# Optimization experiments

Measured on AMD Instinct MI355X. Metric: run time of the kernel, lower is better.

Reference implementation:

```python
import jax, jax.numpy as jnp
import numpy as np

GROUPS = 32
EPS = 1e-6

def groupnorm(x, gamma, beta):
    b, c, h, w = x.shape
    xg = x.reshape(b, GROUPS, c // GROUPS, h, w)
    mean = xg.mean(axis=(2, 3, 4), keepdims=True)
    var = xg.var(axis=(2, 3, 4), keepdims=True)
    xn = ((xg - mean) * jax.lax.rsqrt(var + EPS)).reshape(b, c, h, w)
    return xn * gamma[None, :, None, None] + beta[None, :, None, None]

def conv1x1(x, W, b):
    # x: [b,c,h,w], W: [out,in], b: [out]
    return jnp.einsum('bchw,oc->bohw', x, W) + b[None, :, None, None]

def setup_inputs() -> dict:
    key = jax.random.key(0)
    ks = jax.random.split(key, 12)
    C = 512
    B, H, W = 4, 64, 64
    scale = 1.0 / np.sqrt(C)
    inp = {
        'x': jax.random.normal(ks[0], (B, C, H, W), jnp.float32),
        'mask': jax.random.randint(ks[1], (B, H * W), 0, 2).astype(jnp.float32),
        'gamma': jnp.ones((C,), jnp.float32),
        'beta': jnp.zeros((C,), jnp.float32),
        'Wq': jax.random.normal(ks[2], (C, C), jnp.float32) * scale,
        'bq': jnp.zeros((C,), jnp.float32),
        'Wk': jax.random.normal(ks[3], (C, C), jnp.float32) * scale,
        'bk': jnp.zeros((C,), jnp.float32),
        'Wv': jax.random.normal(ks[4], (C, C), jnp.float32) * scale,
        'bv': jnp.zeros((C,), jnp.float32),
        'Wo': jax.random.normal(ks[5], (C, C), jnp.float32) * scale,
        'bo': jnp.zeros((C,), jnp.float32),
    }
    return inp

def reference(x, mask, gamma, beta, Wq, bq, Wk, bk, Wv, bv, Wo, bo):
    b, c, h, w = x.shape
    hn = groupnorm(x, gamma, beta)
    q = conv1x1(hn, Wq, bq).reshape(b, c, h * w)
    k = conv1x1(hn, Wk, bk).reshape(b, c, h * w)
    v = conv1x1(hn, Wv, bv).reshape(b, c, h * w)
    # scores: [b, hw(query), hw(key)]
    scores = jnp.einsum('bcq,bck->bqk', q, k) * (c ** -0.5)
    attn = jax.nn.softmax(scores, axis=-1)
    # post-softmax multiplicative mask over keys, then renormalize (reweight=True)
    attn = attn * mask[:, None, :]
    attn = attn / jnp.sum(attn, axis=-1, keepdims=True)
    out = jnp.einsum('bck,bqk->bcq', v, attn).reshape(b, c, h, w)
    out = conv1x1(out, Wo, bo)
    return x + out
```

## Files before the change

kernel.cpp:

```cpp
#include <hip/hip_runtime.h>
#include <hip/hip_bf16.h>
#include <stdint.h>

typedef __attribute__((ext_vector_type(4))) float f32x4;
typedef __attribute__((ext_vector_type(16))) float f32x16;
typedef __attribute__((ext_vector_type(4))) int i32x4;
typedef __attribute__((ext_vector_type(8))) int i32x8;
typedef long long ll64;
typedef __attribute__((ext_vector_type(2))) long long ll64x2;

__device__ __forceinline__ float fast_exp2(float x){
#if __has_builtin(__builtin_amdgcn_exp2f)
  return __builtin_amdgcn_exp2f(x);
#else
  return exp2f(x);
#endif
}
__device__ __forceinline__ unsigned char f2fp8(float f){
#if __has_builtin(__builtin_amdgcn_cvt_pk_fp8_f32)
  int r = __builtin_amdgcn_cvt_pk_fp8_f32(f, f, 0, false);
  return (unsigned char)(r & 0xff);
#else
  uint32_t u = __builtin_bit_cast(uint32_t, f);
  uint32_t s = (u >> 24) & 0x80u;
  uint32_t a = u & 0x7fffffffu;
  float af = __builtin_bit_cast(float, a);
  if (af >= 448.f) return (unsigned char)(s | 0x7e);
  a += 0x000fffffu + ((a >> 20) & 1u);
  int e = (int)(a >> 23) - 127;
  if (e < -6) return (unsigned char)s;
  return (unsigned char)(s | (uint32_t)((e + 7) << 3) | ((a >> 20) & 7u));
#endif
}
__device__ __forceinline__ uint32_t pack4(float a, float b, float c, float d){
#if __has_builtin(__builtin_amdgcn_cvt_pk_fp8_f32)
  int lo = __builtin_amdgcn_cvt_pk_fp8_f32(a, b, 0, false);
  int r  = __builtin_amdgcn_cvt_pk_fp8_f32(c, d, lo, true);
  return (uint32_t)r;
#else
  return (uint32_t)f2fp8(a) | ((uint32_t)f2fp8(b) << 8) |
         ((uint32_t)f2fp8(c) << 16) | ((uint32_t)f2fp8(d) << 24);
#endif
}
__device__ __forceinline__ int perm64(int c){
  return (c & ~63) | (((c >> 3) & 3) << 4) | (((c >> 5) & 1) << 3) | (c & 7);
}
__device__ __forceinline__ void gl_lds16b(const unsigned char* g, unsigned char* l){
  __builtin_amdgcn_global_load_lds(
      (const __attribute__((address_space(1))) uint32_t*)g,
      (__attribute__((address_space(3))) uint32_t*)l, 16, 0, 0);
}

__device__ __forceinline__ f32x16 mfma8_32x32x64(i32x8 a, i32x8 b, f32x16 c){
#if __has_builtin(__builtin_amdgcn_mfma_scale_f32_32x32x64_f8f6f4)
  return __builtin_amdgcn_mfma_scale_f32_32x32x64_f8f6f4(a, b, c, 0, 0,
                                                         0, 0x7f7f7f7f, 0, 0x7f7f7f7f);
#else
  ll64x2 al = __builtin_bit_cast(ll64x2, *(i32x4*)&a);
  ll64x2 ah; ah[0] = ((ll64*)&a)[2]; ah[1] = ((ll64*)&a)[3];
  ll64x2 bl = __builtin_bit_cast(ll64x2, *(i32x4*)&b);
  ll64x2 bh; bh[0] = ((ll64*)&b)[2]; bh[1] = ((ll64*)&b)[3];
  c = __builtin_amdgcn_mfma_f32_32x32x16_fp8_fp8(al[0], bl[0], c, 0, 0, 0);
  c = __builtin_amdgcn_mfma_f32_32x32x16_fp8_fp8(al[1], bl[1], c, 0, 0, 0);
  c = __builtin_amdgcn_mfma_f32_32x32x16_fp8_fp8(ah[0], bh[0], c, 0, 0, 0);
  c = __builtin_amdgcn_mfma_f32_32x32x16_fp8_fp8(ah[1], bh[1], c, 0, 0, 0);
  return c;
#endif
}

__global__ __launch_bounds__(256) void k_prep(const float* __restrict__ x,
                                              float* __restrict__ part,
                                              const float* __restrict__ Wq, const float* __restrict__ Wk,
                                              const float* __restrict__ Wv, const float* __restrict__ Wo,
                                              unsigned char* __restrict__ oqk,
                                              unsigned char* __restrict__ ov,
                                              unsigned char* __restrict__ oo){
  __shared__ float red[8];
  const int bid = blockIdx.x;
  if (bid < 1024) {
    const float* p = x + (size_t)bid * 8192;
    float s = 0.f, ss = 0.f;
    for (int i = threadIdx.x; i < 2048; i += 256) {
      float4 v = *(const float4*)(p + (size_t)i * 4);
      s  += v.x + v.y + v.z + v.w;
      ss += v.x*v.x + v.y*v.y + v.z*v.z + v.w*v.w;
    }
    for (int off = 32; off; off >>= 1) { s += __shfl_down(s, off); ss += __shfl_down(ss, off); }
    int w = threadIdx.x >> 6;
    if ((threadIdx.x & 63) == 0) { red[w] = s; red[w + 4] = ss; }
    __syncthreads();
    if (threadIdx.x == 0) {
      part[bid * 2]     = red[0] + red[1] + red[2] + red[3];
      part[bid * 2 + 1] = red[4] + red[5] + red[6] + red[7];
    }
  } else {
    const int cb = bid - 1024;
    const int sel = cb >> 7;
    const float* in = sel == 0 ? Wq : sel == 1 ? Wk : sel == 2 ? Wv : Wo;
    unsigned char* out = sel == 0 ? oqk : sel == 1 ? (oqk + 262144) : sel == 2 ? ov : oo;
    const int i = ((cb & 127) * 256 + threadIdx.x) * 8;
    const int row = i >> 9;
    const int c0  = i & 511;
    float4 v0 = *(const float4*)&in[i];
    float4 v1 = *(const float4*)&in[i + 4];
    unsigned char o[8];
    o[0]=f2fp8(v0.x); o[1]=f2fp8(v0.y); o[2]=f2fp8(v0.z); o[3]=f2fp8(v0.w);
    o[4]=f2fp8(v1.x); o[5]=f2fp8(v1.y); o[6]=f2fp8(v1.z); o[7]=f2fp8(v1.w);
    *(ll64*)&out[row * 512 + perm64(c0)] = *(ll64*)o;
  }
}

__global__ __launch_bounds__(256) void gn_apply(const float* __restrict__ x,
                                                const float* __restrict__ spart,
                                                const float* __restrict__ gamma,
                                                const float* __restrict__ beta,
                                                unsigned char* __restrict__ hn8){
  __shared__ float tile[64][33];
  const int b  = blockIdx.z;
  const int c0 = blockIdx.y * 64;
  const int p0 = blockIdx.x * 32;
  const int t  = threadIdx.x;
  const float* xb = x + (size_t)b * 512 * 4096;
  const int lpx = t & 31, lcc = t >> 5;
#pragma unroll
  for (int i = 0; i < 8; i++)
    tile[lcc + i * 8][lpx] = xb[(size_t)(c0 + lcc + i * 8) * 4096 + p0 + lpx];
  __syncthreads();
  unsigned char* hb = hn8 + (size_t)b * 4096 * 512;
  const int c   = c0 + (t & 31) * 2;
  const int pxi = t >> 5;
  const int g2  = b * 32 + (c >> 4);
  float sum = 0.f, ssum = 0.f;
#pragma unroll
  for (int i = 0; i < 8; i++) { sum += spart[(g2 * 8 + i) * 2]; ssum += spart[(g2 * 8 + i) * 2 + 1]; }
  const float mean = sum * (1.f / 65536.f);
  const float rstd = rsqrtf(ssum * (1.f / 65536.f) - mean * mean + 1e-6f);
  const float ga0 = gamma[c], be0 = beta[c];
  const float ga1 = gamma[c + 1], be1 = beta[c + 1];
  const int cp = perm64(c);
#pragma unroll
  for (int i = 0; i < 4; i++) {
    const int px = pxi + i * 8;
    float v0 = tile[(t & 31) * 2][px];
    float v1 = tile[(t & 31) * 2 + 1][px];
    unsigned int b0 = f2fp8((v0 - mean) * rstd * ga0 + be0);
    unsigned int b1 = f2fp8((v1 - mean) * rstd * ga1 + be1);
    *(unsigned short*)&hb[(size_t)(p0 + px) * 512 + cp] = (unsigned short)(b0 | (b1 << 8));
  }
}

template<int MODE>
__device__ __forceinline__ void gemm8_body(
    int wg, unsigned char* smem,
    const unsigned char* __restrict__ A, const unsigned char* __restrict__ B,
    unsigned char* __restrict__ C8, float* __restrict__ OUTF,
    const float* __restrict__ auxA, const float* __restrict__ auxB,
    const float* __restrict__ partial,
    int K, int ldA, int ldB,
    size_t sA, size_t sB, int gx, int gy)
{
  unsigned char* As = smem;
  unsigned char* Bs = smem + 16384;

  const int bx = wg % gx;
  const int t2 = wg / gx;
  const int by = t2 % gy;
  const int bz = t2 / gy;

  const unsigned char* Ab = A + (size_t)bz * sA;
  const unsigned char* Bb = B + (size_t)bz * sB;
  const int brow = bx * 128;
  const int bcol = by * 128;
  const int t = threadIdx.x;
  const int lane = t & 63;
  const int wid = t >> 6;
  const int wr = wid >> 2;
  const int wc = wid & 3;
  const int l31 = lane & 31;
  const int lh  = lane >> 5;

  f32x16 acc[2];
#pragma unroll
  for (int m = 0; m < 2; m++)
#pragma unroll
    for (int e = 0; e < 16; e++) acc[m][e] = 0.f;

  const unsigned char* srcA1;
  const unsigned char* srcB1;
  {
    const int r = t >> 2, s = (t & 3) ^ ((r >> 1) & 3);
    srcA1 = Ab + (size_t)(brow + r) * ldA + s * 16;
    srcB1 = Bb + (size_t)(bcol + r) * ldB + s * 16;
  }
  auto STAGE = [&](int kt, int buf) {
    const int ko = kt * 64;
    gl_lds16b(srcA1 + ko, &As[buf * 8192 + t * 16]);
    gl_lds16b(srcB1 + ko, &Bs[buf * 8192 + t * 16]);
  };
  auto LDA32 = [&](int buf, int mb) -> i32x8 {
    const int ru = wr * 64 + mb * 32 + l31;
    const int x = (ru >> 1) & 3;
    const unsigned char* base = &As[buf * 8192 + ru * 64];
    i32x4 lo = *(const i32x4*)&base[((2 * lh) ^ x) * 16];
    i32x4 hi = *(const i32x4*)&base[((2 * lh + 1) ^ x) * 16];
    i32x8 r;
    r[0]=lo[0]; r[1]=lo[1]; r[2]=lo[2]; r[3]=lo[3];
    r[4]=hi[0]; r[5]=hi[1]; r[6]=hi[2]; r[7]=hi[3];
    return r;
  };
  auto LDB32 = [&](int buf) -> i32x8 {
    const int ru = wc * 32 + l31;
    const int x = (ru >> 1) & 3;
    const unsigned char* base = &Bs[buf * 8192 + ru * 64];
    i32x4 lo = *(const i32x4*)&base[((2 * lh) ^ x) * 16];
    i32x4 hi = *(const i32x4*)&base[((2 * lh + 1) ^ x) * 16];
    i32x8 r;
    r[0]=lo[0]; r[1]=lo[1]; r[2]=lo[2]; r[3]=lo[3];
    r[4]=hi[0]; r[5]=hi[1]; r[6]=hi[2]; r[7]=hi[3];
    return r;
  };

  const int nk = K >> 6;
  STAGE(0, 0);
  for (int j = 0; j < nk; ++j) {
    const int bi = j & 1;
    asm volatile("s_waitcnt vmcnt(0)" ::: "memory");
    __builtin_amdgcn_s_barrier();
    __builtin_amdgcn_sched_barrier(0);
    if (j + 1 < nk) STAGE(j + 1, bi ^ 1);
    i32x8 aq[2], bq;
    bq = LDB32(bi);
#pragma unroll
    for (int m = 0; m < 2; m++) aq[m] = LDA32(bi, m);
    asm volatile("s_waitcnt lgkmcnt(0)" ::: "memory");
    __builtin_amdgcn_sched_barrier(0);
    __builtin_amdgcn_s_setprio(1);
#pragma unroll
    for (int m = 0; m < 2; m++)
      acc[m] = mfma8_32x32x64(aq[m], bq, acc[m]);
    __builtin_amdgcn_s_setprio(0);
    __builtin_amdgcn_sched_barrier(0);
  }

  const int rowbase = brow + wr * 64;
  const int colbase = bcol + wc * 32;
  const int col = colbase + l31;

  if (MODE == 1) {
    const int tok = col;
#pragma unroll
    for (int mb = 0; mb < 2; mb++)
#pragma unroll
      for (int g = 0; g < 4; g++) {
        const int ch0 = rowbase + mb * 32 + g * 8 + 4 * lh;
        const float* bp = (ch0 < 512) ? (auxA + ch0) : (auxB + ch0 - 512);
        const float4 b4 = *(const float4*)bp;
        unsigned char* dst = C8 + (ch0 < 512 ? 0 : (size_t)8388608);
        const int cp = perm64(ch0 & 511);
        uint32_t w = pack4(acc[mb][g*4+0] + b4.x, acc[mb][g*4+1] + b4.y,
                           acc[mb][g*4+2] + b4.z, acc[mb][g*4+3] + b4.w);
        *(uint32_t*)&dst[(size_t)tok * 512 + cp] = w;
      }
  } else if (MODE == 2) {
    const float bcv = auxA[col];
#pragma unroll
    for (int mb = 0; mb < 2; mb++)
#pragma unroll
      for (int g = 0; g < 4; g++) {
        const int t0 = rowbase + mb * 32 + g * 8 + 4 * lh;
        const int bb = t0 >> 12, p0 = t0 & 4095;
        uint32_t w = pack4(acc[mb][g*4+0] + bcv, acc[mb][g*4+1] + bcv,
                           acc[mb][g*4+2] + bcv, acc[mb][g*4+3] + bcv);
        *(uint32_t*)&C8[((size_t)bb * 512 + col) * 4096 + perm64(p0)] = w;
      }
  } else if (MODE == 4) {
    float* rtmp  = (float*)(smem + 32768);
    float* rinvL = (float*)(smem + 32768 + 2048);
    {
      const int row = t >> 2, q4 = t & 3;
      const float* pb = partial + ((size_t)bz * 32 + q4 * 8) * 4096 + (bcol + row);
      float s = 0.f;
#pragma unroll
      for (int i = 0; i < 8; i++) s += pb[(size_t)i * 4096];
      rtmp[row * 4 + q4] = s;
    }
    __syncthreads();
    if (t < 128) rinvL[t] = 1.f / (rtmp[t * 4] + rtmp[t * 4 + 1] + rtmp[t * 4 + 2] + rtmp[t * 4 + 3]);
    __syncthreads();
    const int ql = wc * 32 + l31;
    const float ri = rinvL[ql];
    const size_t tok = (size_t)bz * 4096 + bcol + ql;
#pragma unroll
    for (int mb = 0; mb < 2; mb++)
#pragma unroll
      for (int g = 0; g < 4; g++) {
        const int c0 = rowbase + mb * 32 + g * 8 + 4 * lh;
        uint32_t w = pack4(acc[mb][g*4+0] * ri, acc[mb][g*4+1] * ri,
                           acc[mb][g*4+2] * ri, acc[mb][g*4+3] * ri);
        *(uint32_t*)&C8[tok * 512 + perm64(c0)] = w;
      }
  } else {
    const float bv = auxB[col];
#pragma unroll
    for (int mb = 0; mb < 2; mb++)
#pragma unroll
      for (int g = 0; g < 4; g++) {
        const int r0 = rowbase + mb * 32 + g * 8 + 4 * lh;
        const int bb = r0 >> 12;
        const int p  = r0 & 4095;
        const size_t idx = ((size_t)bb * 512 + col) * 4096 + p;
        const float4 xv = *(const float4*)&auxA[idx];
        float4 ov;
        ov.x = acc[mb][g * 4 + 0] + xv.x + bv;
        ov.y = acc[mb][g * 4 + 1] + xv.y + bv;
        ov.z = acc[mb][g * 4 + 2] + xv.z + bv;
        ov.w = acc[mb][g * 4 + 3] + xv.w + bv;
        *(float4*)&OUTF[idx] = ov;
      }
  }
}

__global__ __launch_bounds__(512, 2)
void k_qkv(const unsigned char* __restrict__ hn8, const unsigned char* __restrict__ Wqk8,
           const unsigned char* __restrict__ Wv8,
           unsigned char* __restrict__ qk8, unsigned char* __restrict__ vcm8,
           const float* __restrict__ bq, const float* __restrict__ bk,
           const float* __restrict__ bv){
  __shared__ __align__(16) unsigned char SMEM[32768];
  const int lin = blockIdx.x;
  const int nwg = gridDim.x;
  const int wg = ((lin & 7) * (nwg >> 3)) + (lin >> 3);
  if (wg < 1024)
    gemm8_body<1>(wg, SMEM, Wqk8, hn8, qk8, nullptr, bq, bk, nullptr,
                  512, 512, 512, 0, 0, 8, 128);
  else
    gemm8_body<2>(wg - 1024, SMEM, hn8, Wv8, vcm8, nullptr, bv, nullptr, nullptr,
                  512, 512, 512, 0, 0, 128, 4);
}

__global__ __launch_bounds__(512, 2)
void k_pv(const unsigned char* __restrict__ vcm8, const unsigned char* __restrict__ P8,
          unsigned char* __restrict__ ot8, const float* __restrict__ partial){
  __shared__ __align__(16) unsigned char SMEM[32768 + 2560];
  const int lin = blockIdx.x;
  const int nwg = gridDim.x;
  const int wg = ((lin & 7) * (nwg >> 3)) + (lin >> 3);
  gemm8_body<4>(wg, SMEM, vcm8, P8, ot8, nullptr, nullptr, nullptr, partial,
                4096, 4096, 4096,
                (size_t)512 * 4096, (size_t)4096 * 4096, 4, 32);
}
__global__ __launch_bounds__(512, 2)
void k_oproj(const unsigned char* __restrict__ ot8, const unsigned char* __restrict__ Wo8,
             float* __restrict__ out, const float* __restrict__ resid,
             const float* __restrict__ bo){
  __shared__ __align__(16) unsigned char SMEM[32768];
  const int lin = blockIdx.x;
  const int nwg = gridDim.x;
  const int wg = ((lin & 7) * (nwg >> 3)) + (lin >> 3);
  gemm8_body<5>(wg, SMEM, ot8, Wo8, nullptr, out, resid, bo, nullptr,
                512, 512, 512, 0, 0, 128, 4);
}

__global__ __launch_bounds__(512, 2)
void k_scores(const unsigned char* __restrict__ Kt, const unsigned char* __restrict__ Qt,
              unsigned char* __restrict__ C, const float* __restrict__ mask,
              float* __restrict__ partial, float scale,
              size_t sA, size_t sB, size_t sC, int gx, int gy)
{
  __shared__ __align__(16) unsigned char LDSBUF[65536];
  unsigned char* As = LDSBUF;
  unsigned char* Bs = LDSBUF + 32768;

  const int lin = blockIdx.x;
  const int nwg = gridDim.x;
  const int wg = ((lin & 7) * (nwg >> 3)) + (lin >> 3);
  const int bx = wg % gx;
  const int t2 = wg / gx;
  const int by = t2 % gy;
  const int bz = t2 / gy;

  const unsigned char* Ab = Kt + (size_t)bz * sA;
  const unsigned char* Bb = Qt + (size_t)bz * sB;
  const int brow = bx * 256;
  const int bcol = by * 256;
  const int t = threadIdx.x;
  const int lane = t & 63;
  const int wid = t >> 6;
  const int wr = wid >> 2;
  const int wc = wid & 3;
  const int l31 = lane & 31;
  const int lh  = lane >> 5;

  f32x16 acc[4][2];
#pragma unroll
  for (int m = 0; m < 4; m++)
#pragma unroll
    for (int n = 0; n < 2; n++)
#pragma unroll
      for (int e = 0; e < 16; e++) acc[m][n][e] = 0.f;

  const unsigned char* srcA[2];
  const unsigned char* srcB[2];
#pragma unroll
  for (int c = 0; c < 2; ++c) {
    const int q = c * 512 + t, r = q >> 2, s = (q & 3) ^ ((r >> 1) & 3);
    srcA[c] = Ab + (size_t)(brow + r) * 512 + s * 16;
    srcB[c] = Bb + (size_t)(bcol + r) * 512 + s * 16;
  }
  auto STAGE = [&](int kt, int buf) {
    const int ko = kt * 64;
#pragma unroll
    for (int c = 0; c < 2; ++c) {
      gl_lds16b(srcA[c] + ko, &As[buf * 16384 + (c * 512 + t) * 16]);
      gl_lds16b(srcB[c] + ko, &Bs[buf * 16384 + (c * 512 + t) * 16]);
    }
  };
  auto LDA32 = [&](int buf, int mb) -> i32x8 {
    const int ru = wr * 128 + mb * 32 + l31;
    const int x = (ru >> 1) & 3;
    const unsigned char* base = &As[buf * 16384 + ru * 64];
    i32x4 lo = *(const i32x4*)&base[((2 * lh) ^ x) * 16];
    i32x4 hi = *(const i32x4*)&base[((2 * lh + 1) ^ x) * 16];
    i32x8 r;
    r[0]=lo[0]; r[1]=lo[1]; r[2]=lo[2]; r[3]=lo[3];
    r[4]=hi[0]; r[5]=hi[1]; r[6]=hi[2]; r[7]=hi[3];
    return r;
  };
  auto LDB32 = [&](int buf, int nb) -> i32x8 {
    const int ru = wc * 64 + nb * 32 + l31;
    const int x = (ru >> 1) & 3;
    const unsigned char* base = &Bs[buf * 16384 + ru * 64];
    i32x4 lo = *(const i32x4*)&base[((2 * lh) ^ x) * 16];
    i32x4 hi = *(const i32x4*)&base[((2 * lh + 1) ^ x) * 16];
    i32x8 r;
    r[0]=lo[0]; r[1]=lo[1]; r[2]=lo[2]; r[3]=lo[3];
    r[4]=hi[0]; r[5]=hi[1]; r[6]=hi[2]; r[7]=hi[3];
    return r;
  };

  const int nk = 8;
  STAGE(0, 0);
  for (int j = 0; j < nk; ++j) {
    const int bi = j & 1;
    asm volatile("s_waitcnt vmcnt(0)" ::: "memory");
    __builtin_amdgcn_s_barrier();
    __builtin_amdgcn_sched_barrier(0);
    if (j + 1 < nk) STAGE(j + 1, bi ^ 1);
    i32x8 aq[4], bq[2];
#pragma unroll
    for (int n = 0; n < 2; n++) bq[n] = LDB32(bi, n);
#pragma unroll
    for (int m = 0; m < 4; m++) aq[m] = LDA32(bi, m);
    asm volatile("s_waitcnt lgkmcnt(0)" ::: "memory");
    __builtin_amdgcn_sched_barrier(0);
    __builtin_amdgcn_s_setprio(1);
#pragma unroll
    for (int m = 0; m < 4; m++)
#pragma unroll
      for (int n = 0; n < 2; n++)
        acc[m][n] = mfma8_32x32x64(aq[m], bq[n], acc[m][n]);
    __builtin_amdgcn_s_setprio(0);
    __builtin_amdgcn_sched_barrier(0);
  }

  const float* maskb = mask + (size_t)bz * 4096;
  const float sc2 = scale * 1.4426950408889634f;

  asm volatile("s_waitcnt lgkmcnt(0)" ::: "memory");
  __builtin_amdgcn_s_barrier();

  float rs0 = 0.f, rs1 = 0.f;
#pragma unroll
  for (int mi = 0; mi < 4; mi++) {
#pragma unroll
    for (int g = 0; g < 4; g++) {
      const int kl0 = wr * 128 + mi * 32 + g * 8 + 4 * lh;
      const float4 m4 = *(const float4*)&maskb[brow + kl0];
      const int kp = perm64(kl0);
#pragma unroll
      for (int ni = 0; ni < 2; ni++) {
        const int reg = g * 4;
        float v0 = m4.x * fast_exp2(acc[mi][ni][reg + 0] * sc2);
        float v1 = m4.y * fast_exp2(acc[mi][ni][reg + 1] * sc2);
        float v2 = m4.z * fast_exp2(acc[mi][ni][reg + 2] * sc2);
        float v3 = m4.w * fast_exp2(acc[mi][ni][reg + 3] * sc2);
        if (ni == 0) rs0 += v0 + v1 + v2 + v3; else rs1 += v0 + v1 + v2 + v3;
        const int ql = wc * 64 + ni * 32 + l31;
        *(uint32_t*)&LDSBUF[ql * 256 + (kp ^ ((ql & 15) << 4))] = pack4(v0, v1, v2, v3);
      }
    }
  }
  rs0 += __shfl_xor(rs0, 32);
  rs1 += __shfl_xor(rs1, 32);
  if (lh == 0) {
    float* pslot = partial + ((size_t)bz * 32 + (size_t)(bx * 2 + wr)) * 4096;
    pslot[bcol + wc * 64 + l31]      = rs0;
    pslot[bcol + wc * 64 + 32 + l31] = rs1;
  }
  __builtin_amdgcn_s_barrier();
  unsigned char* Cb = C + (size_t)bz * sC;
#pragma unroll
  for (int i = 0; i < 8; i++) {
    const int ch = i * 512 + t;
    const int rl = ch >> 4;
    const int c16 = (ch & 15) * 16;
    i32x4 v = *(const i32x4*)&LDSBUF[rl * 256 + (c16 ^ ((rl & 15) << 4))];
    *(i32x4*)&Cb[(size_t)(bcol + rl) * 4096 + brow + c16] = v;
  }
}

extern "C" void kernel_launch(void* const* d_in, const int* in_sizes, int n_in,
                              void* d_out, int out_size, void* d_ws, size_t ws_size,
                              hipStream_t stream) {
  const float* x     = (const float*)d_in[0];
  const float* mask  = (const float*)d_in[1];
  const float* gamma = (const float*)d_in[2];
  const float* beta  = (const float*)d_in[3];
  const float* Wq    = (const float*)d_in[4];
  const float* bq    = (const float*)d_in[5];
  const float* Wk    = (const float*)d_in[6];
  const float* bk    = (const float*)d_in[7];
  const float* Wv    = (const float*)d_in[8];
  const float* bv    = (const float*)d_in[9];
  const float* Wo    = (const float*)d_in[10];
  const float* bo    = (const float*)d_in[11];
  float* out = (float*)d_out;

  size_t off = 0;
  auto nxt = [&](size_t bytes) -> void* {
    void* p = (char*)d_ws + off;
    off += (bytes + 255) & ~(size_t)255;
    return p;
  };
  float* spart          = (float*)nxt(2048 * sizeof(float));
  float* partial        = (float*)nxt((size_t)4 * 32 * 4096 * 4);
  unsigned char* Wqk8   = (unsigned char*)nxt((size_t)1024 * 512);
  unsigned char* Wv8    = (unsigned char*)nxt((size_t)512 * 512);
  unsigned char* Wo8    = (unsigned char*)nxt((size_t)512 * 512);
  unsigned char* hn8    = (unsigned char*)nxt((size_t)16384 * 512);
  unsigned char* qk8    = (unsigned char*)nxt((size_t)2 * 16384 * 512);
  unsigned char* vcm8   = (unsigned char*)nxt((size_t)4 * 512 * 4096);
  unsigned char* ot8    = (unsigned char*)nxt((size_t)16384 * 512);
  unsigned char* P8     = (unsigned char*)nxt((size_t)4 * 4096 * 4096);

  k_prep<<<1536, 256, 0, stream>>>(x, spart, Wq, Wk, Wv, Wo, Wqk8, Wv8, Wo8);
  gn_apply<<<dim3(128, 8, 4), 256, 0, stream>>>(x, spart, gamma, beta, hn8);
  k_qkv<<<1536, 512, 0, stream>>>(hn8, Wqk8, Wv8, qk8, vcm8, bq, bk, bv);
  k_scores<<<1024, 512, 0, stream>>>(qk8 + (size_t)8388608, qk8, P8, mask, partial,
                                     0.044194173824159216f,
                                     (size_t)4096 * 512, (size_t)4096 * 512,
                                     (size_t)4096 * 4096, 16, 16);
  k_pv<<<512, 512, 0, stream>>>(vcm8, P8, ot8, partial);
  k_oproj<<<512, 512, 0, stream>>>(ot8, Wo8, out, x, bo);
}
```

Measured before the change: 166.6 us.

## Stage GEMM epilogue outputs through LDS for coalesced 16-byte stores

The fp8 GEMM epilogues for QKV, V and PV now write packed results into a swizzled LDS tile. After a barrier, each thread emits one 16-byte row-contiguous global store, replacing scattered 4-byte writes. The output projection swaps its operand order so each lane owns a token column, which makes the fp32 residual read and output write coalesced across lanes. This adds LDS traffic and barriers in the epilogue and relies on the reused shared buffer being free after the main loop.

Measured after the change: 149.4 us (median of 3 runs). 10.3% less time.

```diff
diff --git a/kernel.cpp b/kernel.cpp
--- a/kernel.cpp
+++ b/kernel.cpp
@@ -242,37 +242,57 @@
     __builtin_amdgcn_sched_barrier(0);
   }
 
-  const int rowbase = brow + wr * 64;
-  const int colbase = bcol + wc * 32;
-  const int col = colbase + l31;
+  const int lcol = wc * 32 + l31;
 
   if (MODE == 1) {
-    const int tok = col;
+    asm volatile("s_waitcnt lgkmcnt(0)" ::: "memory");
+    __builtin_amdgcn_s_barrier();
 #pragma unroll
     for (int mb = 0; mb < 2; mb++)
 #pragma unroll
       for (int g = 0; g < 4; g++) {
-        const int ch0 = rowbase + mb * 32 + g * 8 + 4 * lh;
-        const float* bp = (ch0 < 512) ? (auxA + ch0) : (auxB + ch0 - 512);
-        const float4 b4 = *(const float4*)bp;
-        unsigned char* dst = C8 + (ch0 < 512 ? 0 : (size_t)8388608);
-        const int cp = perm64(ch0 & 511);
+        const int lch0 = wr * 64 + mb * 32 + g * 8 + 4 * lh;
+        const int ch0 = brow + lch0;
+        const float4 b4 = *(const float4*)((ch0 < 512) ? (auxA + ch0) : (auxB + ch0 - 512));
+        const int cpL = perm64(lch0 & 127) | (lch0 & 64);
         uint32_t w = pack4(acc[mb][g*4+0] + b4.x, acc[mb][g*4+1] + b4.y,
                            acc[mb][g*4+2] + b4.z, acc[mb][g*4+3] + b4.w);
-        *(uint32_t*)&dst[(size_t)tok * 512 + cp] = w;
+        *(uint32_t*)&smem[lcol * 128 + ((cpL & 127) ^ ((lcol & 7) << 4))] = w;
       }
+    __builtin_amdgcn_s_barrier();
+    unsigned char* dst = C8 + (brow < 512 ? 0 : (size_t)8388608);
+    const int chb = brow & 511;
+#pragma unroll
+    for (int i = 0; i < 2; i++) {
+      const int ch = i * 512 + t;
+      const int rl = ch >> 3, c16 = (ch & 7) * 16;
+      i32x4 v = *(const i32x4*)&smem[rl * 128 + (c16 ^ ((rl & 7) << 4))];
+      *(i32x4*)&dst[(size_t)(bcol + rl) * 512 + chb + c16] = v;
+    }
   } else if (MODE == 2) {
-    const float bcv = auxA[col];
+    const float bcv = auxA[bcol + lcol];
+    asm volatile("s_waitcnt lgkmcnt(0)" ::: "memory");
+    __builtin_amdgcn_s_barrier();
 #pragma unroll
     for (int mb = 0; mb < 2; mb++)
 #pragma unroll
       for (int g = 0; g < 4; g++) {
-        const int t0 = rowbase + mb * 32 + g * 8 + 4 * lh;
-        const int bb = t0 >> 12, p0 = t0 & 4095;
+        const int lt0 = wr * 64 + mb * 32 + g * 8 + 4 * lh;
+        const int ppL = perm64(lt0 & 63) | (lt0 & 64);
         uint32_t w = pack4(acc[mb][g*4+0] + bcv, acc[mb][g*4+1] + bcv,
                            acc[mb][g*4+2] + bcv, acc[mb][g*4+3] + bcv);
-        *(uint32_t*)&C8[((size_t)bb * 512 + col) * 4096 + perm64(p0)] = w;
+        *(uint32_t*)&smem[lcol * 128 + (ppL ^ ((lcol & 7) << 4))] = w;
       }
+    __builtin_amdgcn_s_barrier();
+    const int bb = brow >> 12;
+    const int pb = brow & 4095;
+#pragma unroll
+    for (int i = 0; i < 2; i++) {
+      const int ch = i * 512 + t;
+      const int rl = ch >> 3, c16 = (ch & 7) * 16;
+      i32x4 v = *(const i32x4*)&smem[rl * 128 + (c16 ^ ((rl & 7) << 4))];
+      *(i32x4*)&C8[((size_t)bb * 512 + bcol + rl) * 4096 + pb + c16] = v;
+    }
   } else if (MODE == 4) {
     float* rtmp  = (float*)(smem + 32768);
     float* rinvL = (float*)(smem + 32768 + 2048);
@@ -287,35 +307,41 @@
     __syncthreads();
     if (t < 128) rinvL[t] = 1.f / (rtmp[t * 4] + rtmp[t * 4 + 1] + rtmp[t * 4 + 2] + rtmp[t * 4 + 3]);
     __syncthreads();
-    const int ql = wc * 32 + l31;
-    const float ri = rinvL[ql];
-    const size_t tok = (size_t)bz * 4096 + bcol + ql;
+    const float ri = rinvL[lcol];
 #pragma unroll
     for (int mb = 0; mb < 2; mb++)
 #pragma unroll
       for (int g = 0; g < 4; g++) {
-        const int c0 = rowbase + mb * 32 + g * 8 + 4 * lh;
+        const int lch0 = wr * 64 + mb * 32 + g * 8 + 4 * lh;
+        const int cpL = perm64(lch0 & 63) | (lch0 & 64);
         uint32_t w = pack4(acc[mb][g*4+0] * ri, acc[mb][g*4+1] * ri,
                            acc[mb][g*4+2] * ri, acc[mb][g*4+3] * ri);
-        *(uint32_t*)&C8[tok * 512 + perm64(c0)] = w;
+        *(uint32_t*)&smem[lcol * 128 + (cpL ^ ((lcol & 7) << 4))] = w;
       }
+    __builtin_amdgcn_s_barrier();
+#pragma unroll
+    for (int i = 0; i < 2; i++) {
+      const int ch = i * 512 + t;
+      const int rl = ch >> 3, c16 = (ch & 7) * 16;
+      i32x4 v = *(const i32x4*)&smem[rl * 128 + (c16 ^ ((rl & 7) << 4))];
+      *(i32x4*)&C8[((size_t)bz * 4096 + bcol + rl) * 512 + brow + c16] = v;
+    }
   } else {
-    const float bv = auxB[col];
+    const int tok = bcol + lcol;
+    const int bb = tok >> 12;
+    const int p  = tok & 4095;
 #pragma unroll
     for (int mb = 0; mb < 2; mb++)
 #pragma unroll
       for (int g = 0; g < 4; g++) {
-        const int r0 = rowbase + mb * 32 + g * 8 + 4 * lh;
-        const int bb = r0 >> 12;
-        const int p  = r0 & 4095;
-        const size_t idx = ((size_t)bb * 512 + col) * 4096 + p;
-        const float4 xv = *(const float4*)&auxA[idx];
-        float4 ov;
-        ov.x = acc[mb][g * 4 + 0] + xv.x + bv;
-        ov.y = acc[mb][g * 4 + 1] + xv.y + bv;
-        ov.z = acc[mb][g * 4 + 2] + xv.z + bv;
-        ov.w = acc[mb][g * 4 + 3] + xv.w + bv;
-        *(float4*)&OUTF[idx] = ov;
+        const int ch0 = brow + wr * 64 + mb * 32 + g * 8 + 4 * lh;
+        const float4 b4 = *(const float4*)&auxB[ch0];
+#pragma unroll
+        for (int q = 0; q < 4; q++) {
+          const size_t idx = ((size_t)bb * 512 + ch0 + q) * 4096 + p;
+          OUTF[idx] = acc[mb][g * 4 + q] + auxA[idx] +
+                      (q == 0 ? b4.x : q == 1 ? b4.y : q == 2 ? b4.z : b4.w);
+        }
       }
   }
 }
@@ -350,15 +376,15 @@
                 (size_t)512 * 4096, (size_t)4096 * 4096, 4, 32);
 }
 __global__ __launch_bounds__(512, 2)
-void k_oproj(const unsigned char* __restrict__ ot8, const unsigned char* __restrict__ Wo8,
+void k_oproj(const unsigned char* __restrict__ Wo8, const unsigned char* __restrict__ ot8,
              float* __restrict__ out, const float* __restrict__ resid,
              const float* __restrict__ bo){
   __shared__ __align__(16) unsigned char SMEM[32768];
   const int lin = blockIdx.x;
   const int nwg = gridDim.x;
   const int wg = ((lin & 7) * (nwg >> 3)) + (lin >> 3);
-  gemm8_body<5>(wg, SMEM, ot8, Wo8, nullptr, out, resid, bo, nullptr,
-                512, 512, 512, 0, 0, 128, 4);
+  gemm8_body<5>(wg, SMEM, Wo8, ot8, nullptr, out, resid, bo, nullptr,
+                512, 512, 512, 0, 0, 4, 128);
 }
 
 __global__ __launch_bounds__(512, 2)
@@ -551,5 +577,5 @@
                                      (size_t)4096 * 512, (size_t)4096 * 512,
                                      (size_t)4096 * 4096, 16, 16);
   k_pv<<<512, 512, 0, stream>>>(vcm8, P8, ot8, partial);
-  k_oproj<<<512, 512, 0, stream>>>(ot8, Wo8, out, x, bo);
-}
+  k_oproj<<<512, 512, 0, stream>>>(Wo8, ot8, out, x, bo);
+}
```
